# Performance work log

Hardware: AMD Instinct MI355X
Metric: run time of the kernel (lower is better)

## Reference

```python
import jax, jax.numpy as jnp
import numpy as np

B, L, E = 512, 50, 512
VOCAB = 32000
EPS = 1e-5


def setup_inputs() -> dict:
    key = jax.random.key(0)
    ks = jax.random.split(key, 16)
    inp = {
        'src_tokens': jax.random.randint(ks[0], (B, L), 0, VOCAB, dtype=jnp.int32),
        'trg_tokens': jax.random.randint(ks[1], (B, L), 0, VOCAB, dtype=jnp.int32),
        'pad_idx': 1,
        'emb_src': jax.random.normal(ks[2], (VOCAB, E), jnp.float32) * 0.02,
        'emb_trg': jax.random.normal(ks[3], (VOCAB, E), jnp.float32) * 0.02,
        'W1': jax.random.normal(ks[4], (20, E), jnp.float32) / np.sqrt(E),  # Conv1d(1,20,k=E) kernel squeezed
        'b1': jax.random.normal(ks[5], (20,), jnp.float32) * 0.01,
        'g1': jnp.ones((20,), jnp.float32),
        'beta1': jnp.zeros((20,), jnp.float32),
        'W2': jax.random.normal(ks[6], (40, 20, 3, 3), jnp.float32) / np.sqrt(20 * 9),
        'b2': jax.random.normal(ks[7], (40,), jnp.float32) * 0.01,
        'g2': jnp.ones((40,), jnp.float32),
        'beta2': jnp.zeros((40,), jnp.float32),
        'Wfc1': jax.random.normal(ks[8], (20, 40 * 11 * 11), jnp.float32) / np.sqrt(40 * 11 * 11),
        'bfc1': jnp.zeros((20,), jnp.float32),
        'Wfc2': jax.random.normal(ks[9], (1, 20), jnp.float32) / np.sqrt(20),
        'bfc2': jnp.zeros((1,), jnp.float32),
    }
    return inp


def _maxpool2(x):  # [B,C,H,W] -> 2x2/2 valid max pool
    return jax.lax.reduce_window(x, -jnp.inf, jax.lax.max, (1, 1, 2, 2), (1, 1, 2, 2), 'VALID')


def reference(src_tokens, trg_tokens, pad_idx, emb_src, emb_trg, W1, b1, g1, beta1,
              W2, b2, g2, beta2, Wfc1, bfc1, Wfc2, bfc2):
    src_e = emb_src[src_tokens]  # [B,L,E]
    trg_e = emb_trg[trg_tokens]  # [B,L,E]

    def conv1_bn_relu(x):
        # per-sample Conv1d(1,20,k=E): collapses E -> scalar per position/channel
        f = jnp.einsum('ble,ce->blc', x, W1) + b1  # [B,L,20]
        # per-sample BatchNorm1d in training mode: stats over the L positions of each sample
        mu = jnp.mean(f, axis=1, keepdims=True)
        var = jnp.var(f, axis=1, keepdims=True)  # biased, as torch uses for normalization
        f = (f - mu) * jax.lax.rsqrt(var + EPS) * g1 + beta1
        return jax.nn.relu(f)

    s = conv1_bn_relu(src_e)  # [B,L,20]
    t = conv1_bn_relu(trg_e)  # [B,L,20]

    # broadcast outer-sum: out[b,i,j,c] = s[b,j,c] + t[b,i,c]
    out = s[:, None, :, :] + t[:, :, None, :]          # [B,L,L,20]
    out = jnp.transpose(out, (0, 3, 1, 2))             # [B,20,L,L]
    out = _maxpool2(out)                                # [B,20,25,25]

    out = jax.lax.conv_general_dilated(out, W2, (1, 1), 'VALID') + b2[None, :, None, None]  # [B,40,23,23]
    # BatchNorm2d training mode: stats over (batch, H, W)
    mu = jnp.mean(out, axis=(0, 2, 3), keepdims=True)
    var = jnp.var(out, axis=(0, 2, 3), keepdims=True)
    out = (out - mu) * jax.lax.rsqrt(var + EPS) * g2[None, :, None, None] + beta2[None, :, None, None]
    out = jax.nn.relu(out)
    out = _maxpool2(out)                                # [B,40,11,11]

    out = out.reshape(out.shape[0], -1)                 # [B,4840]
    out = out @ Wfc1.T + bfc1
    out = out @ Wfc2.T + bfc2
    return jax.nn.sigmoid(out)                          # [B,1]
```

## Files before the change

### kernel.cpp

```cpp
#include <hip/hip_runtime.h>
#include <hip/hip_bf16.h>

#define EPS 1e-5f

typedef __attribute__((ext_vector_type(8)))  short bf16x8;
typedef __attribute__((ext_vector_type(16))) float f32x16;

__device__ __forceinline__ float bf2f(unsigned short u) {
  union { unsigned int i; float f; } x; x.i = ((unsigned int)u) << 16; return x.f;
}
__device__ __forceinline__ float loadp(const void* p, int i, bool f32) {
  return f32 ? ((const float*)p)[i] : bf2f(((const unsigned short*)p)[i]);
}
__device__ __forceinline__ bool detect_f32(const void* g1) {
  return ((const unsigned int*)g1)[0] == 0x3F800000u;
}

__global__ __launch_bounds__(256) void k0_prep(
    const void* __restrict__ W1, const void* __restrict__ W2,
    const void* __restrict__ Wfc1,
    const void* __restrict__ g1, const void* __restrict__ beta1,
    const void* __restrict__ g2, const void* __restrict__ beta2,
    const void* __restrict__ bfc1, const void* __restrict__ Wfc2,
    const void* __restrict__ bfc2,
    float* __restrict__ W1T, float* __restrict__ WT, float* __restrict__ WS,
    float* __restrict__ Wfc1T, float* __restrict__ prm,
    unsigned short* __restrict__ BpG)
{
  const bool f32 = detect_f32(g1);
  int g = blockIdx.x * 256 + threadIdx.x;
  const int NT = 64 * 256;
  for (int i = g; i < 512 * 20; i += NT) {
    int e = i / 20, c = i - e * 20;
    W1T[i] = loadp(W1, c * 512 + e, f32);
  }
  const unsigned short* W1u = (const unsigned short*)W1;
  for (int i = g; i < 2048; i += NT) {
    int s = i >> 6, lane = i & 63;
    int n = lane & 31, hk = lane >> 5;
#pragma unroll
    for (int j = 0; j < 8; ++j) {
      int e = s * 16 + hk * 8 + j;
      BpG[i * 8 + j] = (n < 20) ? W1u[n * 512 + e] : (unsigned short)0;
    }
  }
  for (int i = g; i < 40 * 3 * 20; i += NT) {
    int o = i / 60, r = i - o * 60;
    int k = r / 20, c = r - k * 20;
    float st = 0.f, ss = 0.f;
    for (int q = 0; q < 3; ++q) {
      st += loadp(W2, ((o * 20 + c) * 3 + k) * 3 + q, f32);
      ss += loadp(W2, ((o * 20 + c) * 3 + q) * 3 + k, f32);
    }
    WT[(o * 3 + k) * 20 + c] = st;
    WS[(o * 3 + k) * 20 + c] = ss;
  }
  for (int i = g; i < 4840 * 20; i += NT) {
    int kk = i / 4840, idx = i - kk * 4840;
    Wfc1T[idx * 20 + kk] = loadp(Wfc1, i, f32);
  }
  if (g < 20)        prm[g] = loadp(g1,    g,       f32);
  else if (g < 40)   prm[g] = loadp(beta1, g - 20,  f32);
  else if (g < 80)   prm[g] = loadp(g2,    g - 40,  f32);
  else if (g < 120)  prm[g] = loadp(beta2, g - 80,  f32);
  else if (g < 140)  prm[g] = loadp(bfc1,  g - 120, f32);
  else if (g < 160)  prm[g] = loadp(Wfc2,  g - 140, f32);
  else if (g == 160) prm[g] = loadp(bfc2,  0,       f32);
}

__global__ __launch_bounds__(256) void k1_vocab(
    const void* __restrict__ emb_src, const void* __restrict__ emb_trg,
    const void* __restrict__ g1flag,
    const float* __restrict__ W1T,
    const unsigned short* __restrict__ BpG,
    unsigned short* __restrict__ F)
{
  __shared__ unsigned short Blds[32 * 64 * 8];
  __shared__ float part[4][64][21];
  const bool f32 = detect_f32(g1flag);
  int t = threadIdx.x;
  int lane = t & 63;
  int wv = __builtin_amdgcn_readfirstlane(t >> 6);

  if (!f32) {
    {
      const uint4* srcp = (const uint4*)BpG;
      uint4* dstp = (uint4*)Blds;
      for (int i = t; i < 2048; i += 256) dstp[i] = srcp[i];
    }
    int m = lane & 31, half = lane >> 5;
    int grow = blockIdx.x * 128 + wv * 32 + m;
    int table = grow >= 32000;
    int v = grow - table * 32000;
    const unsigned short* arow =
        (const unsigned short*)(table ? emb_trg : emb_src) + (size_t)v * 512 + half * 8;
    uint4 a[32];
#pragma unroll
    for (int s = 0; s < 32; ++s) a[s] = *(const uint4*)(arow + s * 16);
    __syncthreads();
    f32x16 acc;
#pragma unroll
    for (int r = 0; r < 16; ++r) acc[r] = 0.f;
#pragma unroll
    for (int s = 0; s < 32; ++s) {
      union { uint4 u; bf16x8 h; } af, bf;
      af.u = a[s];
      bf.u = *(const uint4*)(Blds + ((size_t)s * 64 + lane) * 8);
      acc = __builtin_amdgcn_mfma_f32_32x32x16_bf16(af.h, bf.h, acc, 0, 0, 0);
    }
    int col = lane & 31;
    if (col < 20) {
      int rbase = blockIdx.x * 128 + wv * 32 + 4 * half;
#pragma unroll
      for (int r = 0; r < 16; ++r) {
        int row = rbase + (r & 3) + 8 * (r >> 2);
        F[(size_t)row * 24 + col] =
            (unsigned short)(__bfloat16_as_ushort(__float2bfloat16(acc[r])));
      }
    }
  } else {
    int slot = lane;
    int grow = blockIdx.x * 64 + slot;
    for (int pass = 0; pass < 2; ++pass) {
      int gr = blockIdx.x * 128 + pass * 64 + slot;
      int table = gr >= 32000;
      int v = gr - table * 32000;
      const float4* rowp = (const float4*)((const float*)(table ? emb_trg : emb_src) +
                                           (size_t)v * 512 + wv * 128);
      float acc[20];
#pragma unroll
      for (int c = 0; c < 20; ++c) acc[c] = 0.f;
      for (int outer = 0; outer < 4; ++outer) {
        float4 u[8];
#pragma unroll
        for (int q = 0; q < 8; ++q) u[q] = rowp[outer * 8 + q];
#pragma unroll
        for (int q = 0; q < 8; ++q) {
          float vv[4] = { u[q].x, u[q].y, u[q].z, u[q].w };
          const float* w = W1T + (wv * 128 + outer * 32 + q * 4) * 20;
#pragma unroll
          for (int j = 0; j < 4; ++j)
#pragma unroll
            for (int c = 0; c < 20; ++c) acc[c] = fmaf(vv[j], w[j * 20 + c], acc[c]);
        }
      }
      float* pp = &part[wv][slot][0];
#pragma unroll
      for (int c = 0; c < 20; ++c) pp[c] = acc[c];
      __syncthreads();
      for (int i = t; i < 1280; i += 256) {
        int row = i / 20, c = i - row * 20;
        float val = part[0][row][c] + part[1][row][c] + part[2][row][c] + part[3][row][c];
        F[(size_t)(blockIdx.x * 128 + pass * 64 + row) * 24 + c] =
            (unsigned short)(__bfloat16_as_ushort(__float2bfloat16(val)));
      }
      __syncthreads();
    }
  }
}

__global__ __launch_bounds__(256) void k2_sample(
    const int* __restrict__ src_tok, const int* __restrict__ trg_tok,
    const unsigned short* __restrict__ F,
    const float* __restrict__ WT, const float* __restrict__ WS,
    const float* __restrict__ prm,
    float* __restrict__ C1, float* __restrict__ R, float* __restrict__ S2)
{
  __shared__ float fl[1000];
  __shared__ float wl[2400];
  __shared__ float pmax[500];
  __shared__ float convl[40 * 24];
  __shared__ float sc[20], sh[20];
  __shared__ int tokl[50];
  int bb = blockIdx.x;
  int side = bb >> 9, b = bb & 511;
  int t = threadIdx.x;
  if (t < 50) tokl[t] = side ? trg_tok[b * 50 + t] : src_tok[b * 50 + t];
  const float* wsrc = side ? WT : WS;
  for (int i = t; i < 2400; i += 256) wl[i] = wsrc[i];
  __syncthreads();
  if (t < 250) {
    int l = t / 5, j = t - (t / 5) * 5;
    const unsigned short* fr = F + (size_t)(side * 32000 + tokl[l]) * 24 + j * 4;
    uint2 u = *(const uint2*)fr;
    union { unsigned int i; float f; } e0, e1, e2, e3;
    e0.i = u.x << 16; e1.i = u.x & 0xffff0000u;
    e2.i = u.y << 16; e3.i = u.y & 0xffff0000u;
    float* dst = &fl[l * 20 + j * 4];
    dst[0] = e0.f; dst[1] = e1.f; dst[2] = e2.f; dst[3] = e3.f;
  }
  __syncthreads();
  if (t < 20) {
    float s = 0.f, s2 = 0.f;
#pragma unroll
    for (int l = 0; l < 50; ++l) { float v = fl[l * 20 + t]; s += v; s2 += v * v; }
    float mu = s * (1.0f / 50.0f);
    float var = s2 * (1.0f / 50.0f) - mu * mu;
    float k = prm[t] * rsqrtf(var + EPS);
    sc[t] = k; sh[t] = prm[20 + t] - k * mu;
  }
  __syncthreads();
  for (int i = t; i < 500; i += 256) {
    int p = i / 20, c = i - p * 20;
    float k = sc[c], s0 = sh[c];
    float v0 = fmaxf(k * fl[(2 * p) * 20 + c] + s0, 0.f);
    float v1 = fmaxf(k * fl[(2 * p + 1) * 20 + c] + s0, 0.f);
    pmax[i] = fmaxf(v0, v1);
  }
  __syncthreads();
  for (int i = t; i < 920; i += 256) {
    int o = i / 23, y = i - o * 23;
    float a = 0.f;
#pragma unroll
    for (int ky = 0; ky < 3; ++ky) {
      const float* wr = &wl[(o * 3 + ky) * 20];
      const float* pr = &pmax[(y + ky) * 20];
#pragma unroll
      for (int c = 0; c < 20; ++c) a = fmaf(wr[c], pr[c], a);
    }
    C1[((size_t)o * 1024 + bb) * 23 + y] = a;
    convl[o * 24 + y] = a;
  }
  __syncthreads();
  if (t < 40) {
    float s = 0.f, s2 = 0.f;
#pragma unroll
    for (int y = 0; y < 23; ++y) { float v = convl[t * 24 + y]; s += v; s2 += v * v; }
    R[t * 1024 + bb] = s;
    S2[t * 1024 + bb] = s2;
  }
}

__global__ __launch_bounds__(256) void k3_bn2(
    const float* __restrict__ R, const float* __restrict__ S2,
    const float* __restrict__ prm,
    float* __restrict__ bn2)
{
  int o = blockIdx.x, t = threadIdx.x;
  float s1a = 0, s2a = 0, s1b = 0, s2b = 0, sab = 0;
  for (int b = t; b < 512; b += 256) {
    float ra = R[o * 1024 + 512 + b], rb = R[o * 1024 + b];
    s1a += ra; s1b += rb; sab += ra * rb;
    s2a += S2[o * 1024 + 512 + b];
    s2b += S2[o * 1024 + b];
  }
  __shared__ float Rd[5][256];
  Rd[0][t] = s1a; Rd[1][t] = s2a; Rd[2][t] = s1b; Rd[3][t] = s2b; Rd[4][t] = sab;
  __syncthreads();
  for (int s = 128; s > 0; s >>= 1) {
    if (t < s) {
#pragma unroll
      for (int q = 0; q < 5; ++q) Rd[q][t] += Rd[q][t + s];
    }
    __syncthreads();
  }
  if (t == 0) {
    const float invN = 1.0f / (512.0f * 23.0f);
    float muA = Rd[0][0] * invN, muB = Rd[2][0] * invN;
    float ea2 = Rd[1][0] * invN - muA * muA;
    float eb2 = Rd[3][0] * invN - muB * muB;
    float cross = 2.0f * (Rd[4][0] * (1.0f / (529.0f * 512.0f)) - muA * muB);
    float var = ea2 + eb2 + cross;
    float k = prm[40 + o] * rsqrtf(var + EPS);
    bn2[o] = k;
    bn2[40 + o] = prm[80 + o] - k * (muA + muB);
  }
}

__global__ __launch_bounds__(256) void k4_fc(
    const float* __restrict__ C1,
    const float* __restrict__ bn2,
    const float* __restrict__ Wfc1T,
    const float* __restrict__ prm,
    const void* __restrict__ g1flag,
    void* __restrict__ outv)
{
  const bool f32 = detect_f32(g1flag);
  int b = blockIdx.x, t = threadIdx.x;
  __shared__ float mA[440], mB[440];
  __shared__ float k2s[40], c2s[40];
  __shared__ float red[20][256];
  __shared__ float o1[20];
  if (t < 40) k2s[t] = bn2[t];
  else if (t < 80) c2s[t - 40] = bn2[t];
  __syncthreads();
  for (int i = t; i < 440; i += 256) {
    int o = i / 11, y = i - o * 11;
    const float* pa = C1 + ((size_t)o * 1024 + 512 + b) * 23;
    const float* pb = C1 + ((size_t)o * 1024 + b) * 23;
    float a0 = pa[2 * y], a1 = pa[2 * y + 1];
    float b0 = pb[2 * y], b1 = pb[2 * y + 1];
    if (k2s[o] >= 0.f) { mA[i] = fmaxf(a0, a1); mB[i] = fmaxf(b0, b1); }
    else               { mA[i] = fminf(a0, a1); mB[i] = fminf(b0, b1); }
  }
  __syncthreads();
  float acc[20];
#pragma unroll
  for (int c = 0; c < 20; ++c) acc[c] = 0.f;
  for (int idx = t; idx < 4840; idx += 256) {
    int o = idx / 121, r = idx - o * 121;
    int y = r / 11, x = r - y * 11;
    float p = fmaxf(k2s[o] * (mA[o * 11 + y] + mB[o * 11 + x]) + c2s[o], 0.f);
    const float* w = Wfc1T + idx * 20;
#pragma unroll
    for (int c = 0; c < 20; ++c) acc[c] = fmaf(p, w[c], acc[c]);
  }
#pragma unroll
  for (int c = 0; c < 20; ++c) red[c][t] = acc[c];
  __syncthreads();
  for (int s = 128; s > 0; s >>= 1) {
    if (t < s) {
#pragma unroll
      for (int c = 0; c < 20; ++c) red[c][t] += red[c][t + s];
    }
    __syncthreads();
  }
  if (t < 20) o1[t] = red[t][0] + prm[120 + t];
  __syncthreads();
  if (t == 0) {
    float z = prm[160];
#pragma unroll
    for (int c = 0; c < 20; ++c) z = fmaf(prm[140 + c], o1[c], z);
    float sg = 1.0f / (1.0f + expf(-z));
    if (f32) ((float*)outv)[b] = sg;
    else     ((__hip_bfloat16*)outv)[b] = __float2bfloat16(sg);
  }
}

extern "C" void kernel_launch(void* const* d_in, const int* in_sizes, int n_in,
                              void* d_out, int out_size, void* d_ws, size_t ws_size,
                              hipStream_t stream) {
  const int* src_tok = (const int*)d_in[0];
  const int* trg_tok = (const int*)d_in[1];
  const void* emb_src = d_in[3];
  const void* emb_trg = d_in[4];
  const void* W1    = d_in[5];
  const void* g1    = d_in[7];
  const void* beta1 = d_in[8];
  const void* W2    = d_in[9];
  const void* g2    = d_in[11];
  const void* beta2 = d_in[12];
  const void* Wfc1  = d_in[13];
  const void* bfc1  = d_in[14];
  const void* Wfc2  = d_in[15];
  const void* bfc2  = d_in[16];

  char* ws = (char*)d_ws;
  float* W1T          = (float*)(ws + 0);
  float* WT           = (float*)(ws + 40960);
  float* WS           = (float*)(ws + 50560);
  float* Wfc1T        = (float*)(ws + 60160);
  float* prm          = (float*)(ws + 447360);
  float* bn2          = (float*)(ws + 448384);
  float* R            = (float*)(ws + 448896);
  float* S2           = (float*)(ws + 612736);
  unsigned short* BpG = (unsigned short*)(ws + 776576);
  unsigned short* F   = (unsigned short*)(ws + 809344);
  float* C1           = (float*)(ws + 3881344);

  k0_prep<<<64, 256, 0, stream>>>(W1, W2, Wfc1, g1, beta1, g2, beta2, bfc1, Wfc2,
                                  bfc2, W1T, WT, WS, Wfc1T, prm, BpG);
  k1_vocab<<<500, 256, 0, stream>>>(emb_src, emb_trg, g1, W1T, BpG, F);
  k2_sample<<<1024, 256, 0, stream>>>(src_tok, trg_tok, F, WT, WS, prm, C1, R, S2);
  k3_bn2<<<40, 256, 0, stream>>>(R, S2, prm, bn2);
  k4_fc<<<512, 256, 0, stream>>>(C1, bn2, Wfc1T, prm, g1, d_out);
}
```

Before: 225.5 us.

## Split vocab projection over K across waves with smaller blocks and LDS reduction

The vocab projection kernel now gives each block 32 rows instead of 128 and launches four times as many blocks. The four waves each take one quarter of the K dimension, and their partial sums are reduced through LDS. Embedding rows are loaded with coalesced full-row reads and staged in padded LDS, while B fragments go straight to registers instead of being copied to LDS first. This aims to raise occupancy and memory parallelism on the bandwidth-bound embedding read, at the cost of an extra LDS reduction pass and more barriers.

```diff
diff --git a/kernel.cpp b/kernel.cpp
--- a/kernel.cpp
+++ b/kernel.cpp
@@ -8,6 +8,9 @@
 
 __device__ __forceinline__ float bf2f(unsigned short u) {
   union { unsigned int i; float f; } x; x.i = ((unsigned int)u) << 16; return x.f;
+}
+__device__ __forceinline__ unsigned short f2bf(float v) {
+  return (unsigned short)__bfloat16_as_ushort(__float2bfloat16(v));
 }
 __device__ __forceinline__ float loadp(const void* p, int i, bool f32) {
   return f32 ? ((const float*)p)[i] : bf2f(((const unsigned short*)p)[i]);
@@ -75,61 +78,64 @@
     const unsigned short* __restrict__ BpG,
     unsigned short* __restrict__ F)
 {
-  __shared__ unsigned short Blds[32 * 64 * 8];
-  __shared__ float part[4][64][21];
+  __shared__ __align__(16) char ldsbuf[33280];
+  unsigned short* Alds = (unsigned short*)ldsbuf;
+  float* part = (float*)ldsbuf;
   const bool f32 = detect_f32(g1flag);
   int t = threadIdx.x;
   int lane = t & 63;
   int wv = __builtin_amdgcn_readfirstlane(t >> 6);
+  int rowbase = blockIdx.x * 32;
+  int table = rowbase >= 32000;
+  int vbase = rowbase - table * 32000;
 
   if (!f32) {
-    {
-      const uint4* srcp = (const uint4*)BpG;
-      uint4* dstp = (uint4*)Blds;
-      for (int i = t; i < 2048; i += 256) dstp[i] = srcp[i];
-    }
-    int m = lane & 31, half = lane >> 5;
-    int grow = blockIdx.x * 128 + wv * 32 + m;
-    int table = grow >= 32000;
-    int v = grow - table * 32000;
-    const unsigned short* arow =
-        (const unsigned short*)(table ? emb_trg : emb_src) + (size_t)v * 512 + half * 8;
-    uint4 a[32];
-#pragma unroll
-    for (int s = 0; s < 32; ++s) a[s] = *(const uint4*)(arow + s * 16);
+    const unsigned short* emb = (const unsigned short*)(table ? emb_trg : emb_src);
+    uint4 av[8];
+#pragma unroll
+    for (int r = 0; r < 8; ++r)
+      av[r] = *(const uint4*)(emb + (size_t)(vbase + wv * 8 + r) * 512 + lane * 8);
+    uint4 bv[8];
+#pragma unroll
+    for (int s = 0; s < 8; ++s)
+      bv[s] = *(const uint4*)(BpG + ((size_t)(wv * 8 + s) * 64 + lane) * 8);
+#pragma unroll
+    for (int r = 0; r < 8; ++r)
+      *(uint4*)(Alds + (wv * 8 + r) * 520 + lane * 8) = av[r];
     __syncthreads();
     f32x16 acc;
 #pragma unroll
     for (int r = 0; r < 16; ++r) acc[r] = 0.f;
-#pragma unroll
-    for (int s = 0; s < 32; ++s) {
+    const unsigned short* abase = Alds + (lane & 31) * 520 + wv * 128 + (lane >> 5) * 8;
+#pragma unroll
+    for (int s = 0; s < 8; ++s) {
       union { uint4 u; bf16x8 h; } af, bf;
-      af.u = a[s];
-      bf.u = *(const uint4*)(Blds + ((size_t)s * 64 + lane) * 8);
+      af.u = *(const uint4*)(abase + s * 16);
+      bf.u = bv[s];
       acc = __builtin_amdgcn_mfma_f32_32x32x16_bf16(af.h, bf.h, acc, 0, 0, 0);
     }
-    int col = lane & 31;
-    if (col < 20) {
-      int rbase = blockIdx.x * 128 + wv * 32 + 4 * half;
-#pragma unroll
-      for (int r = 0; r < 16; ++r) {
-        int row = rbase + (r & 3) + 8 * (r >> 2);
-        F[(size_t)row * 24 + col] =
-            (unsigned short)(__bfloat16_as_ushort(__float2bfloat16(acc[r])));
+    __syncthreads();
+    float* pp = part + ((size_t)wv * 64 + lane) * 17;
+#pragma unroll
+    for (int r = 0; r < 16; ++r) pp[r] = acc[r];
+    __syncthreads();
+    for (int i = t; i < 1024; i += 256) {
+      int ln = i & 63, reg = i >> 6;
+      float v = part[(0 * 64 + ln) * 17 + reg] + part[(1 * 64 + ln) * 17 + reg] +
+                part[(2 * 64 + ln) * 17 + reg] + part[(3 * 64 + ln) * 17 + reg];
+      int col = ln & 31;
+      if (col < 20) {
+        int row = (reg & 3) + 8 * (reg >> 2) + 4 * (ln >> 5);
+        F[(size_t)(rowbase + row) * 24 + col] = f2bf(v);
       }
     }
   } else {
-    int slot = lane;
-    int grow = blockIdx.x * 64 + slot;
-    for (int pass = 0; pass < 2; ++pass) {
-      int gr = blockIdx.x * 128 + pass * 64 + slot;
-      int table = gr >= 32000;
-      int v = gr - table * 32000;
-      const float4* rowp = (const float4*)((const float*)(table ? emb_trg : emb_src) +
-                                           (size_t)v * 512 + wv * 128);
-      float acc[20];
-#pragma unroll
-      for (int c = 0; c < 20; ++c) acc[c] = 0.f;
+    float fa[20];
+#pragma unroll
+    for (int c = 0; c < 20; ++c) fa[c] = 0.f;
+    if (lane < 32) {
+      const float* emb = (const float*)(table ? emb_trg : emb_src);
+      const float4* rowp = (const float4*)(emb + (size_t)(vbase + lane) * 512 + wv * 128);
       for (int outer = 0; outer < 4; ++outer) {
         float4 u[8];
 #pragma unroll
@@ -141,20 +147,22 @@
 #pragma unroll
           for (int j = 0; j < 4; ++j)
 #pragma unroll
-            for (int c = 0; c < 20; ++c) acc[c] = fmaf(vv[j], w[j * 20 + c], acc[c]);
+            for (int c = 0; c < 20; ++c) fa[c] = fmaf(vv[j], w[j * 20 + c], fa[c]);
         }
       }
-      float* pp = &part[wv][slot][0];
-#pragma unroll
-      for (int c = 0; c < 20; ++c) pp[c] = acc[c];
-      __syncthreads();
-      for (int i = t; i < 1280; i += 256) {
-        int row = i / 20, c = i - row * 20;
-        float val = part[0][row][c] + part[1][row][c] + part[2][row][c] + part[3][row][c];
-        F[(size_t)(blockIdx.x * 128 + pass * 64 + row) * 24 + c] =
-            (unsigned short)(__bfloat16_as_ushort(__float2bfloat16(val)));
-      }
-      __syncthreads();
+    }
+    __syncthreads();
+    if (lane < 32) {
+      float* pp = part + ((size_t)wv * 32 + lane) * 21;
+#pragma unroll
+      for (int c = 0; c < 20; ++c) pp[c] = fa[c];
+    }
+    __syncthreads();
+    for (int i = t; i < 640; i += 256) {
+      int row = i / 20, c = i - row * 20;
+      float v = part[(0 * 32 + row) * 21 + c] + part[(1 * 32 + row) * 21 + c] +
+                part[(2 * 32 + row) * 21 + c] + part[(3 * 32 + row) * 21 + c];
+      F[(size_t)(rowbase + row) * 24 + c] = f2bf(v);
     }
   }
 }
@@ -360,7 +368,7 @@
 
   k0_prep<<<64, 256, 0, stream>>>(W1, W2, Wfc1, g1, beta1, g2, beta2, bfc1, Wfc2,
                                   bfc2, W1T, WT, WS, Wfc1T, prm, BpG);
-  k1_vocab<<<500, 256, 0, stream>>>(emb_src, emb_trg, g1, W1T, BpG, F);
+  k1_vocab<<<2000, 256, 0, stream>>>(emb_src, emb_trg, g1, W1T, BpG, F);
   k2_sample<<<1024, 256, 0, stream>>>(src_tok, trg_tok, F, WT, WS, prm, C1, R, S2);
   k3_bn2<<<40, 256, 0, stream>>>(R, S2, prm, bn2);
   k4_fc<<<512, 256, 0, stream>>>(C1, bn2, Wfc1T, prm, g1, d_out);
```

New measurement: 225.6 us. Within noise of the previous version (+0.0%).
